# Kernel optimization log

Hardware: AMD Instinct MI355X
Metric: run time of the kernel (lower is better)

The kernel has to match this reference:

```python
import jax, jax.numpy as jnp
import numpy as np

B, T, H = 32, 512, 512
NUM_LAYERS = 2  # outer modules; each nn.GRU itself has NUM_LAYERS internal layers
TOTAL = NUM_LAYERS * NUM_LAYERS  # 4 actual recurrent layers
EPS = 1e-5


def setup_inputs() -> dict:
    key = jax.random.key(0)
    ks = jax.random.split(key, 8)
    s = 1.0 / np.sqrt(H)
    x = jax.random.normal(ks[0], (B, T, H), dtype=jnp.float32)
    # descending lengths in [1, T] (enforce_sorted=True in torch)
    seq_lens = jnp.sort(jax.random.randint(ks[1], (B,), 1, T + 1))[::-1]
    Wih = jax.random.uniform(ks[2], (TOTAL, 3 * H, H), minval=-s, maxval=s)
    Whh = jax.random.uniform(ks[3], (TOTAL, 3 * H, H), minval=-s, maxval=s)
    bih = jax.random.uniform(ks[4], (TOTAL, 3 * H), minval=-s, maxval=s)
    bhh = jax.random.uniform(ks[5], (TOTAL, 3 * H), minval=-s, maxval=s)
    gamma = jnp.ones((NUM_LAYERS, H), jnp.float32)
    beta = jnp.zeros((NUM_LAYERS, H), jnp.float32)
    return {"x": x, "Wih": Wih, "Whh": Whh, "bih": bih, "bhh": bhh,
            "gamma": gamma, "beta": beta, "seq_lens": seq_lens}


def _gru_layer(x, wih, whh, bi, bh):
    # x: [B,T,I]; torch GRU equations (gate order r,z,n)
    xi = jnp.einsum('bti,gi->btg', x, wih) + bi  # [B,T,3H]

    def step(h, xt):
        hh = h @ whh.T + bh
        xr, xz, xn = jnp.split(xt, 3, axis=-1)
        hr, hz, hn = jnp.split(hh, 3, axis=-1)
        r = jax.nn.sigmoid(xr + hr)
        z = jax.nn.sigmoid(xz + hz)
        n = jnp.tanh(xn + r * hn)
        h = (1 - z) * n + z * h
        return h, h

    h0 = jnp.zeros((x.shape[0], whh.shape[1]), x.dtype)
    _, ys = jax.lax.scan(step, h0, jnp.swapaxes(xi, 0, 1))  # [T,B,H]
    return jnp.swapaxes(ys, 0, 1)


def _layernorm(x, g, b):
    mu = jnp.mean(x, axis=-1, keepdims=True)
    var = jnp.mean(jnp.square(x - mu), axis=-1, keepdims=True)
    return (x - mu) * jax.lax.rsqrt(var + EPS) * g + b


def reference(x, Wih, Whh, bih, bhh, gamma, beta, seq_lens):
    # pack_padded_sequence semantics (unidirectional): outputs at valid steps
    # t < len match the full-sequence run; padded steps become zeros after
    # pad_packed_sequence, then LayerNorm is applied to the whole padded tensor.
    mask = (jnp.arange(T)[None, :] < seq_lens[:, None])[:, :, None]  # [B,T,1]
    out = x
    idx = 0
    for l in range(NUM_LAYERS):
        for _k in range(NUM_LAYERS):  # each nn.GRU has NUM_LAYERS internal layers
            out = _gru_layer(out, Wih[idx], Whh[idx], bih[idx], bhh[idx])
            idx += 1
        out = jnp.where(mask, out, 0.0)
        out = _layernorm(out, gamma[l], beta[l])
    return out
```

## Files before the change

### kernel.cpp

```cpp
#include <hip/hip_runtime.h>

typedef unsigned short ushort_t;
typedef __attribute__((ext_vector_type(8))) short short8;
typedef __attribute__((ext_vector_type(4))) float f32x4;

#define B_ 32
#define T_ 512
#define H_ 512
#define CH_ 16

__device__ __forceinline__ float bf2f(ushort_t u) {
  union { unsigned int i; float f; } v; v.i = ((unsigned int)u) << 16; return v.f;
}
__device__ __forceinline__ ushort_t f2bf(float f) {
  union { float fv; unsigned int i; } v; v.fv = f;
  unsigned int x = v.i;
  x += 0x7fffu + ((x >> 16) & 1u);
  return (ushort_t)(x >> 16);
}

__device__ __forceinline__ void poll_row(const int* row, int nf) {
  const int lane = threadIdx.x & 63;
  for (;;) {
    int v = 1;
    if (lane < nf)
      v = __hip_atomic_load(row + lane, __ATOMIC_RELAXED, __HIP_MEMORY_SCOPE_AGENT);
    if (__all(v != 0)) break;
    __builtin_amdgcn_s_sleep(1);
  }
  asm volatile("" ::: "memory");
}

__global__ void prep_w(const float* __restrict__ Wih, const float* __restrict__ Whh,
                       ushort_t* __restrict__ WihBf, ushort_t* __restrict__ WhhBf) {
  int i = blockIdx.x * 256 + threadIdx.x;
  WihBf[i] = f2bf(Wih[i]);
  WhhBf[i] = f2bf(Whh[i]);
}

__global__ void prep_x(const float* __restrict__ x, ushort_t* __restrict__ xA) {
  int i = blockIdx.x * 256 + threadIdx.x;
  int h  = i & (H_ - 1);
  int tb = i >> 9;
  int b  = tb & (B_ - 1);
  int t  = tb >> 5;
  xA[i] = f2bf(x[((size_t)b * T_ + t) * H_ + h]);
}

__device__ void gru_stage(
    const ushort_t* __restrict__ xin, ushort_t* __restrict__ xout,
    const ushort_t* __restrict__ Wih, const ushort_t* __restrict__ Whh,
    const float* __restrict__ bih, const float* __restrict__ bhh,
    ushort_t* __restrict__ hbuf,
    int* __restrict__ selfFl,
    const int* __restrict__ prodFl,
    int prodN, int wg,
    float (*Gx)[33], float (*Gh)[33], float (*hprev)[B_])
{
  const int tid   = threadIdx.x;
  const int lane  = tid & 63;
  const int wave  = tid >> 6;
  const int jb    = wg * CH_;
  const int m16   = lane & 15;
  const int quad  = lane >> 4;
  const int bcol  = (wave & 1) * 16 + m16;

  hprev[tid >> 5][tid & 31]       = 0.0f;
  hprev[8 + (tid >> 5)][tid & 31] = 0.0f;

  const ushort_t* Wsel = (wave < 2) ? Wih : Whh;
  short8 afrag[3][16];
#pragma unroll
  for (int g = 0; g < 3; ++g) {
    const ushort_t* wp = Wsel + (size_t)(g * H_ + jb + m16) * H_ + quad * 8;
#pragma unroll
    for (int kk = 0; kk < 16; ++kk)
      afrag[g][kk] = *(const short8*)(wp + kk * 32);
  }

  const int b0 = tid & 31;
  const int c  = tid >> 5;
  const int c0 = 2 * c, c1 = 2 * c + 1;
  const float bxr0 = bih[0*H_ + jb + c0], bhr0 = bhh[0*H_ + jb + c0];
  const float bxz0 = bih[1*H_ + jb + c0], bhz0 = bhh[1*H_ + jb + c0];
  const float bxn0 = bih[2*H_ + jb + c0], bhn0 = bhh[2*H_ + jb + c0];
  const float bxr1 = bih[0*H_ + jb + c1], bhr1 = bhh[0*H_ + jb + c1];
  const float bxz1 = bih[1*H_ + jb + c1], bhz1 = bhh[1*H_ + jb + c1];
  const float bxn1 = bih[2*H_ + jb + c1], bhn1 = bhh[2*H_ + jb + c1];

  __syncthreads();

  for (int s = 0; s < T_; ++s) {
    f32x4 acc0 = {0.f, 0.f, 0.f, 0.f};
    f32x4 acc1 = acc0, acc2 = acc0;

    if (wave < 2) {
      const ushort_t* src = xin + ((size_t)s * B_ + bcol) * H_ + quad * 8;
      if (prodFl) {
        poll_row(prodFl + s * 32, prodN);
#pragma unroll
        for (int kk = 0; kk < 16; ++kk) {
          const unsigned long long* p = (const unsigned long long*)(src + kk * 32);
          unsigned long long lo = __hip_atomic_load(p,     __ATOMIC_RELAXED, __HIP_MEMORY_SCOPE_AGENT);
          unsigned long long hi = __hip_atomic_load(p + 1, __ATOMIC_RELAXED, __HIP_MEMORY_SCOPE_AGENT);
          union { unsigned long long q[2]; short8 v; } u; u.q[0] = lo; u.q[1] = hi;
          acc0 = __builtin_amdgcn_mfma_f32_16x16x32_bf16(afrag[0][kk], u.v, acc0, 0, 0, 0);
          acc1 = __builtin_amdgcn_mfma_f32_16x16x32_bf16(afrag[1][kk], u.v, acc1, 0, 0, 0);
          acc2 = __builtin_amdgcn_mfma_f32_16x16x32_bf16(afrag[2][kk], u.v, acc2, 0, 0, 0);
        }
      } else {
#pragma unroll
        for (int kk = 0; kk < 16; ++kk) {
          short8 bf = *(const short8*)(src + kk * 32);
          acc0 = __builtin_amdgcn_mfma_f32_16x16x32_bf16(afrag[0][kk], bf, acc0, 0, 0, 0);
          acc1 = __builtin_amdgcn_mfma_f32_16x16x32_bf16(afrag[1][kk], bf, acc1, 0, 0, 0);
          acc2 = __builtin_amdgcn_mfma_f32_16x16x32_bf16(afrag[2][kk], bf, acc2, 0, 0, 0);
        }
      }
    } else {
      if (s > 0) poll_row(selfFl + (s - 1) * 32, 32);
      const ushort_t* src = hbuf + ((size_t)(s & 1) * B_ + bcol) * H_ + quad * 8;
#pragma unroll
      for (int kk = 0; kk < 16; ++kk) {
        const unsigned long long* p = (const unsigned long long*)(src + kk * 32);
        unsigned long long lo = __hip_atomic_load(p,     __ATOMIC_RELAXED, __HIP_MEMORY_SCOPE_AGENT);
        unsigned long long hi = __hip_atomic_load(p + 1, __ATOMIC_RELAXED, __HIP_MEMORY_SCOPE_AGENT);
        union { unsigned long long q[2]; short8 v; } u; u.q[0] = lo; u.q[1] = hi;
        acc0 = __builtin_amdgcn_mfma_f32_16x16x32_bf16(afrag[0][kk], u.v, acc0, 0, 0, 0);
        acc1 = __builtin_amdgcn_mfma_f32_16x16x32_bf16(afrag[1][kk], u.v, acc1, 0, 0, 0);
        acc2 = __builtin_amdgcn_mfma_f32_16x16x32_bf16(afrag[2][kk], u.v, acc2, 0, 0, 0);
      }
    }

    float (*Gd)[33] = (wave < 2) ? Gx : Gh;
#pragma unroll
    for (int r = 0; r < 4; ++r) {
      Gd[ 0 + quad * 4 + r][bcol] = acc0[r];
      Gd[16 + quad * 4 + r][bcol] = acc1[r];
      Gd[32 + quad * 4 + r][bcol] = acc2[r];
    }
    __syncthreads();

    ushort_t* hdst = hbuf + (size_t)((s + 1) & 1) * B_ * H_;
    float hv0, hv1;
    {
      float rr = 1.f / (1.f + __expf(-(Gx[c0][b0] + bxr0 + Gh[c0][b0] + bhr0)));
      float zz = 1.f / (1.f + __expf(-(Gx[16 + c0][b0] + bxz0 + Gh[16 + c0][b0] + bhz0)));
      float nn = tanhf(Gx[32 + c0][b0] + bxn0 + rr * (Gh[32 + c0][b0] + bhn0));
      hv0 = (1.f - zz) * nn + zz * hprev[c0][b0];
      hprev[c0][b0] = hv0;
    }
    {
      float rr = 1.f / (1.f + __expf(-(Gx[c1][b0] + bxr1 + Gh[c1][b0] + bhr1)));
      float zz = 1.f / (1.f + __expf(-(Gx[16 + c1][b0] + bxz1 + Gh[16 + c1][b0] + bhz1)));
      float nn = tanhf(Gx[32 + c1][b0] + bxn1 + rr * (Gh[32 + c1][b0] + bhn1));
      hv1 = (1.f - zz) * nn + zz * hprev[c1][b0];
      hprev[c1][b0] = hv1;
    }
    unsigned int pack = (unsigned int)f2bf(hv0) | ((unsigned int)f2bf(hv1) << 16);
    __hip_atomic_store((unsigned int*)(hdst + (size_t)b0 * H_ + jb + c0), pack,
                       __ATOMIC_RELAXED, __HIP_MEMORY_SCOPE_AGENT);
    __hip_atomic_store((unsigned int*)(xout + ((size_t)s * B_ + b0) * H_ + jb + c0), pack,
                       __ATOMIC_RELAXED, __HIP_MEMORY_SCOPE_AGENT);

    asm volatile("s_waitcnt vmcnt(0)" ::: "memory");
    __syncthreads();
    if (tid == 0)
      __hip_atomic_store(selfFl + s * 32 + wg, 1,
                         __ATOMIC_RELAXED, __HIP_MEMORY_SCOPE_AGENT);
  }
}

__device__ void ln_stage(
    const ushort_t* __restrict__ xin,
    ushort_t* __restrict__ xout_bf,
    float* __restrict__ out_f32,
    const float* __restrict__ gamma, const float* __restrict__ beta,
    const int* __restrict__ seq,
    int* __restrict__ selfFl, const int* __restrict__ prodFl, int prodN, int wg)
{
  const int lane = threadIdx.x & 63;
  const int wv   = threadIdx.x >> 6;
  const int b    = wg * 4 + wv;
  const int len  = seq[b];
  const int h0   = lane * 8;

  float g[8], be[8];
#pragma unroll
  for (int j = 0; j < 8; ++j) { g[j] = gamma[h0 + j]; be[j] = beta[h0 + j]; }

  for (int s = 0; s < T_; ++s) {
    poll_row(prodFl + s * 32, prodN);
    const unsigned long long* p =
        (const unsigned long long*)(xin + ((size_t)s * B_ + b) * H_ + h0);
    unsigned long long lo = __hip_atomic_load(p,     __ATOMIC_RELAXED, __HIP_MEMORY_SCOPE_AGENT);
    unsigned long long hi = __hip_atomic_load(p + 1, __ATOMIC_RELAXED, __HIP_MEMORY_SCOPE_AGENT);
    union { unsigned long long q[2]; ushort_t u[8]; } un; un.q[0] = lo; un.q[1] = hi;
    const bool valid = s < len;
    float v[8];
#pragma unroll
    for (int j = 0; j < 8; ++j) v[j] = valid ? bf2f(un.u[j]) : 0.f;

    float sum = 0.f, sq = 0.f;
#pragma unroll
    for (int j = 0; j < 8; ++j) { sum += v[j]; sq += v[j] * v[j]; }
#pragma unroll
    for (int off = 32; off > 0; off >>= 1) {
      sum += __shfl_xor(sum, off);
      sq  += __shfl_xor(sq, off);
    }
    float mu   = sum * (1.f / H_);
    float var  = sq * (1.f / H_) - mu * mu;
    float rstd = rsqrtf(var + 1e-5f);

    if (xout_bf) {
      union { unsigned long long q[2]; ushort_t u[8]; } o;
#pragma unroll
      for (int j = 0; j < 8; ++j)
        o.u[j] = f2bf((v[j] - mu) * rstd * g[j] + be[j]);
      unsigned long long* q =
          (unsigned long long*)(xout_bf + ((size_t)s * B_ + b) * H_ + h0);
      __hip_atomic_store(q,     o.q[0], __ATOMIC_RELAXED, __HIP_MEMORY_SCOPE_AGENT);
      __hip_atomic_store(q + 1, o.q[1], __ATOMIC_RELAXED, __HIP_MEMORY_SCOPE_AGENT);
      asm volatile("s_waitcnt vmcnt(0)" ::: "memory");
      __syncthreads();
      if (threadIdx.x == 0)
        __hip_atomic_store(selfFl + s * 32 + wg, 1,
                           __ATOMIC_RELAXED, __HIP_MEMORY_SCOPE_AGENT);
    } else {
      float* dst = out_f32 + ((size_t)b * T_ + s) * H_ + h0;
#pragma unroll
      for (int j = 0; j < 8; ++j)
        dst[j] = (v[j] - mu) * rstd * g[j] + be[j];
    }
  }
}

__global__ __launch_bounds__(256, 1) void gru_mega(
    ushort_t* __restrict__ xA, ushort_t* __restrict__ xB,
    ushort_t* __restrict__ xC, ushort_t* __restrict__ xD,
    const ushort_t* __restrict__ WihBf, const ushort_t* __restrict__ WhhBf,
    const float* __restrict__ bih, const float* __restrict__ bhh,
    const float* __restrict__ gamma, const float* __restrict__ beta,
    const int* __restrict__ seq,
    ushort_t* __restrict__ hbase, int* __restrict__ flbase,
    float* __restrict__ out)
{
  __shared__ float Gx[48][33];
  __shared__ float Gh[48][33];
  __shared__ float hprev[CH_][B_];

  const int bid = blockIdx.x;
  const int FS = T_ * 32;
  int* fl0   = flbase;
  int* fl1   = flbase + 1 * FS;
  int* flln0 = flbase + 2 * FS;
  int* fl2   = flbase + 3 * FS;
  int* fl3   = flbase + 4 * FS;
  const int WM = 3 * H_ * H_;
  const int HB = 2 * B_ * H_;

  if (bid < 32) {
    gru_stage(xA, xB, WihBf, WhhBf, bih, bhh,
              hbase, fl0, nullptr, 0, bid, Gx, Gh, hprev);
  } else if (bid < 64) {
    gru_stage(xB, xC, WihBf + WM, WhhBf + WM, bih + 1536, bhh + 1536,
              hbase + HB, fl1, fl0, 32, bid - 32, Gx, Gh, hprev);
  } else if (bid < 72) {
    ln_stage(xC, xD, nullptr, gamma, beta, seq, flln0, fl1, 32, bid - 64);
  } else if (bid < 104) {
    gru_stage(xD, xA, WihBf + 2 * WM, WhhBf + 2 * WM, bih + 2 * 1536, bhh + 2 * 1536,
              hbase + 2 * HB, fl2, flln0, 8, bid - 72, Gx, Gh, hprev);
  } else if (bid < 136) {
    gru_stage(xA, xB, WihBf + 3 * WM, WhhBf + 3 * WM, bih + 3 * 1536, bhh + 3 * 1536,
              hbase + 3 * HB, fl3, fl2, 32, bid - 104, Gx, Gh, hprev);
  } else {
    ln_stage(xB, nullptr, out, gamma + H_, beta + H_, seq,
             nullptr, fl3, 32, bid - 136);
  }
}

#define WIH_OFF 0u
#define WHH_OFF 6291456u
#define XA_OFF  12582912u
#define XB_OFF  29360128u
#define XC_OFF  46137344u
#define XD_OFF  62914560u
#define HB_OFF  79691776u
#define FL_OFF  79953920u

extern "C" void kernel_launch(void* const* d_in, const int* in_sizes, int n_in,
                              void* d_out, int out_size, void* d_ws, size_t ws_size,
                              hipStream_t stream) {
  (void)in_sizes; (void)n_in; (void)out_size; (void)ws_size;
  const float* x     = (const float*)d_in[0];
  const float* Wih   = (const float*)d_in[1];
  const float* Whh   = (const float*)d_in[2];
  const float* bih   = (const float*)d_in[3];
  const float* bhh   = (const float*)d_in[4];
  const float* gamma = (const float*)d_in[5];
  const float* beta  = (const float*)d_in[6];
  const int*   seq   = (const int*)d_in[7];

  char* ws = (char*)d_ws;
  ushort_t* WihBf = (ushort_t*)(ws + WIH_OFF);
  ushort_t* WhhBf = (ushort_t*)(ws + WHH_OFF);
  ushort_t* xA    = (ushort_t*)(ws + XA_OFF);
  ushort_t* xB    = (ushort_t*)(ws + XB_OFF);
  ushort_t* xC    = (ushort_t*)(ws + XC_OFF);
  ushort_t* xD    = (ushort_t*)(ws + XD_OFF);
  ushort_t* hbase = (ushort_t*)(ws + HB_OFF);
  int*      flags = (int*)(ws + FL_OFF);

  hipMemsetAsync(ws + HB_OFF, 0, 262144 + 327680, stream);

  prep_w<<<3145728 / 256, 256, 0, stream>>>(Wih, Whh, WihBf, WhhBf);
  prep_x<<<8388608 / 256, 256, 0, stream>>>(x, xA);

  gru_mega<<<144, 256, 0, stream>>>(xA, xB, xC, xD, WihBf, WhhBf,
                                    bih, bhh, gamma, beta, seq,
                                    hbase, flags, (float*)d_out);
}
```

Before: 4.343 ms.

## Replace block barrier with per-wave flags, batched coherent loads, fast gate math

Each wave now publishes its own completion flag, so the end-of-step __syncthreads is gone and consumers poll 128 flags per step. The shared gate buffers are double-buffered so the next step's writes cannot race the current readers. Producer and recurrent-state reads are issued as 16 batched sc0/sc1 dwordx4 loads, waited on once, instead of pairs of 64-bit atomic loads. Sigmoid and tanh use rcp-based fast approximations, and the hidden state stays in registers. Intermediate buffers are reused to drop one activation buffer, at the cost of more flag memory and slightly less accurate activations.

```diff
diff --git a/kernel.cpp b/kernel.cpp
--- a/kernel.cpp
+++ b/kernel.cpp
@@ -19,14 +19,40 @@
   return (ushort_t)(x >> 16);
 }
 
+__device__ __forceinline__ float fsig(float a) {
+  return __builtin_amdgcn_rcpf(1.f + __expf(-a));
+}
+__device__ __forceinline__ float ftanh(float a) {
+  return 1.f - 2.f * __builtin_amdgcn_rcpf(1.f + __expf(2.f * a));
+}
+
+__device__ __forceinline__ void cload16(short8& dst, const ushort_t* p) {
+  asm volatile("global_load_dwordx4 %0, %1, off sc0 sc1"
+               : "=v"(dst) : "v"(p) : "memory");
+}
+__device__ __forceinline__ void cstore16(const short8& v, ushort_t* p) {
+  asm volatile("global_store_dwordx4 %1, %0, off sc0 sc1"
+               :: "v"(v), "v"(p) : "memory");
+}
+#define WAIT_VM0 asm volatile("s_waitcnt vmcnt(0)" ::: "memory")
+__device__ __forceinline__ void vfence(short8& v) { asm volatile("" : "+v"(v)); }
+
 __device__ __forceinline__ void poll_row(const int* row, int nf) {
   const int lane = threadIdx.x & 63;
-  for (;;) {
-    int v = 1;
-    if (lane < nf)
-      v = __hip_atomic_load(row + lane, __ATOMIC_RELAXED, __HIP_MEMORY_SCOPE_AGENT);
-    if (__all(v != 0)) break;
-    __builtin_amdgcn_s_sleep(1);
+  if (nf > 64) {
+    for (;;) {
+      int a = __hip_atomic_load(row + lane,      __ATOMIC_RELAXED, __HIP_MEMORY_SCOPE_AGENT);
+      int b = __hip_atomic_load(row + 64 + lane, __ATOMIC_RELAXED, __HIP_MEMORY_SCOPE_AGENT);
+      if (__all(a != 0 && b != 0)) break;
+      __builtin_amdgcn_s_sleep(1);
+    }
+  } else {
+    for (;;) {
+      int a = (lane < nf)
+            ? __hip_atomic_load(row + lane, __ATOMIC_RELAXED, __HIP_MEMORY_SCOPE_AGENT) : 1;
+      if (__all(a != 0)) break;
+      __builtin_amdgcn_s_sleep(1);
+    }
   }
   asm volatile("" ::: "memory");
 }
@@ -37,7 +63,6 @@
   WihBf[i] = f2bf(Wih[i]);
   WhhBf[i] = f2bf(Whh[i]);
 }
-
 __global__ void prep_x(const float* __restrict__ x, ushort_t* __restrict__ xA) {
   int i = blockIdx.x * 256 + threadIdx.x;
   int h  = i & (H_ - 1);
@@ -55,7 +80,7 @@
     int* __restrict__ selfFl,
     const int* __restrict__ prodFl,
     int prodN, int wg,
-    float (*Gx)[33], float (*Gh)[33], float (*hprev)[B_])
+    float (*Gbuf)[2][48][33])
 {
   const int tid   = threadIdx.x;
   const int lane  = tid & 63;
@@ -64,9 +89,6 @@
   const int m16   = lane & 15;
   const int quad  = lane >> 4;
   const int bcol  = (wave & 1) * 16 + m16;
-
-  hprev[tid >> 5][tid & 31]       = 0.0f;
-  hprev[8 + (tid >> 5)][tid & 31] = 0.0f;
 
   const ushort_t* Wsel = (wave < 2) ? Wih : Whh;
   short8 afrag[3][16];
@@ -87,26 +109,27 @@
   const float bxr1 = bih[0*H_ + jb + c1], bhr1 = bhh[0*H_ + jb + c1];
   const float bxz1 = bih[1*H_ + jb + c1], bhz1 = bhh[1*H_ + jb + c1];
   const float bxn1 = bih[2*H_ + jb + c1], bhn1 = bhh[2*H_ + jb + c1];
-
-  __syncthreads();
+  float hp0 = 0.f, hp1 = 0.f;
 
   for (int s = 0; s < T_; ++s) {
+    const int p = s & 1;
     f32x4 acc0 = {0.f, 0.f, 0.f, 0.f};
     f32x4 acc1 = acc0, acc2 = acc0;
 
     if (wave < 2) {
       const ushort_t* src = xin + ((size_t)s * B_ + bcol) * H_ + quad * 8;
       if (prodFl) {
-        poll_row(prodFl + s * 32, prodN);
+        poll_row(prodFl + s * prodN, prodN);
+        short8 bfr[16];
+#pragma unroll
+        for (int kk = 0; kk < 16; ++kk) cload16(bfr[kk], src + kk * 32);
+        WAIT_VM0;
 #pragma unroll
         for (int kk = 0; kk < 16; ++kk) {
-          const unsigned long long* p = (const unsigned long long*)(src + kk * 32);
-          unsigned long long lo = __hip_atomic_load(p,     __ATOMIC_RELAXED, __HIP_MEMORY_SCOPE_AGENT);
-          unsigned long long hi = __hip_atomic_load(p + 1, __ATOMIC_RELAXED, __HIP_MEMORY_SCOPE_AGENT);
-          union { unsigned long long q[2]; short8 v; } u; u.q[0] = lo; u.q[1] = hi;
-          acc0 = __builtin_amdgcn_mfma_f32_16x16x32_bf16(afrag[0][kk], u.v, acc0, 0, 0, 0);
-          acc1 = __builtin_amdgcn_mfma_f32_16x16x32_bf16(afrag[1][kk], u.v, acc1, 0, 0, 0);
-          acc2 = __builtin_amdgcn_mfma_f32_16x16x32_bf16(afrag[2][kk], u.v, acc2, 0, 0, 0);
+          vfence(bfr[kk]);
+          acc0 = __builtin_amdgcn_mfma_f32_16x16x32_bf16(afrag[0][kk], bfr[kk], acc0, 0, 0, 0);
+          acc1 = __builtin_amdgcn_mfma_f32_16x16x32_bf16(afrag[1][kk], bfr[kk], acc1, 0, 0, 0);
+          acc2 = __builtin_amdgcn_mfma_f32_16x16x32_bf16(afrag[2][kk], bfr[kk], acc2, 0, 0, 0);
         }
       } else {
 #pragma unroll
@@ -118,21 +141,22 @@
         }
       }
     } else {
-      if (s > 0) poll_row(selfFl + (s - 1) * 32, 32);
-      const ushort_t* src = hbuf + ((size_t)(s & 1) * B_ + bcol) * H_ + quad * 8;
+      if (s > 0) poll_row(selfFl + (s - 1) * 128, 128);
+      const ushort_t* src = hbuf + ((size_t)p * B_ + bcol) * H_ + quad * 8;
+      short8 bfr[16];
+#pragma unroll
+      for (int kk = 0; kk < 16; ++kk) cload16(bfr[kk], src + kk * 32);
+      WAIT_VM0;
 #pragma unroll
       for (int kk = 0; kk < 16; ++kk) {
-        const unsigned long long* p = (const unsigned long long*)(src + kk * 32);
-        unsigned long long lo = __hip_atomic_load(p,     __ATOMIC_RELAXED, __HIP_MEMORY_SCOPE_AGENT);
-        unsigned long long hi = __hip_atomic_load(p + 1, __ATOMIC_RELAXED, __HIP_MEMORY_SCOPE_AGENT);
-        union { unsigned long long q[2]; short8 v; } u; u.q[0] = lo; u.q[1] = hi;
-        acc0 = __builtin_amdgcn_mfma_f32_16x16x32_bf16(afrag[0][kk], u.v, acc0, 0, 0, 0);
-        acc1 = __builtin_amdgcn_mfma_f32_16x16x32_bf16(afrag[1][kk], u.v, acc1, 0, 0, 0);
-        acc2 = __builtin_amdgcn_mfma_f32_16x16x32_bf16(afrag[2][kk], u.v, acc2, 0, 0, 0);
+        vfence(bfr[kk]);
+        acc0 = __builtin_amdgcn_mfma_f32_16x16x32_bf16(afrag[0][kk], bfr[kk], acc0, 0, 0, 0);
+        acc1 = __builtin_amdgcn_mfma_f32_16x16x32_bf16(afrag[1][kk], bfr[kk], acc1, 0, 0, 0);
+        acc2 = __builtin_amdgcn_mfma_f32_16x16x32_bf16(afrag[2][kk], bfr[kk], acc2, 0, 0, 0);
       }
     }
 
-    float (*Gd)[33] = (wave < 2) ? Gx : Gh;
+    float (*Gd)[33] = Gbuf[p][(wave < 2) ? 0 : 1];
 #pragma unroll
     for (int r = 0; r < 4; ++r) {
       Gd[ 0 + quad * 4 + r][bcol] = acc0[r];
@@ -141,32 +165,30 @@
     }
     __syncthreads();
 
-    ushort_t* hdst = hbuf + (size_t)((s + 1) & 1) * B_ * H_;
-    float hv0, hv1;
+    float (*Gx)[33] = Gbuf[p][0];
+    float (*Gh)[33] = Gbuf[p][1];
+    ushort_t* hdst = hbuf + (size_t)(p ^ 1) * B_ * H_;
     {
-      float rr = 1.f / (1.f + __expf(-(Gx[c0][b0] + bxr0 + Gh[c0][b0] + bhr0)));
-      float zz = 1.f / (1.f + __expf(-(Gx[16 + c0][b0] + bxz0 + Gh[16 + c0][b0] + bhz0)));
-      float nn = tanhf(Gx[32 + c0][b0] + bxn0 + rr * (Gh[32 + c0][b0] + bhn0));
-      hv0 = (1.f - zz) * nn + zz * hprev[c0][b0];
-      hprev[c0][b0] = hv0;
+      float rr = fsig(Gx[c0][b0] + bxr0 + Gh[c0][b0] + bhr0);
+      float zz = fsig(Gx[16 + c0][b0] + bxz0 + Gh[16 + c0][b0] + bhz0);
+      float nn = ftanh(Gx[32 + c0][b0] + bxn0 + rr * (Gh[32 + c0][b0] + bhn0));
+      hp0 = (1.f - zz) * nn + zz * hp0;
     }
     {
-      float rr = 1.f / (1.f + __expf(-(Gx[c1][b0] + bxr1 + Gh[c1][b0] + bhr1)));
-      float zz = 1.f / (1.f + __expf(-(Gx[16 + c1][b0] + bxz1 + Gh[16 + c1][b0] + bhz1)));
-      float nn = tanhf(Gx[32 + c1][b0] + bxn1 + rr * (Gh[32 + c1][b0] + bhn1));
-      hv1 = (1.f - zz) * nn + zz * hprev[c1][b0];
-      hprev[c1][b0] = hv1;
-    }
-    unsigned int pack = (unsigned int)f2bf(hv0) | ((unsigned int)f2bf(hv1) << 16);
+      float rr = fsig(Gx[c1][b0] + bxr1 + Gh[c1][b0] + bhr1);
+      float zz = fsig(Gx[16 + c1][b0] + bxz1 + Gh[16 + c1][b0] + bhz1);
+      float nn = ftanh(Gx[32 + c1][b0] + bxn1 + rr * (Gh[32 + c1][b0] + bhn1));
+      hp1 = (1.f - zz) * nn + zz * hp1;
+    }
+    unsigned int pack = (unsigned int)f2bf(hp0) | ((unsigned int)f2bf(hp1) << 16);
     __hip_atomic_store((unsigned int*)(hdst + (size_t)b0 * H_ + jb + c0), pack,
                        __ATOMIC_RELAXED, __HIP_MEMORY_SCOPE_AGENT);
     __hip_atomic_store((unsigned int*)(xout + ((size_t)s * B_ + b0) * H_ + jb + c0), pack,
                        __ATOMIC_RELAXED, __HIP_MEMORY_SCOPE_AGENT);
 
-    asm volatile("s_waitcnt vmcnt(0)" ::: "memory");
-    __syncthreads();
-    if (tid == 0)
-      __hip_atomic_store(selfFl + s * 32 + wg, 1,
+    WAIT_VM0;
+    if (lane == 0)
+      __hip_atomic_store(selfFl + s * 128 + wg * 4 + wave, 1,
                          __ATOMIC_RELAXED, __HIP_MEMORY_SCOPE_AGENT);
   }
 }
@@ -177,7 +199,8 @@
     float* __restrict__ out_f32,
     const float* __restrict__ gamma, const float* __restrict__ beta,
     const int* __restrict__ seq,
-    int* __restrict__ selfFl, const int* __restrict__ prodFl, int prodN, int wg)
+    int* __restrict__ selfFl,
+    const int* __restrict__ prodFl, int prodN, int wg)
 {
   const int lane = threadIdx.x & 63;
   const int wv   = threadIdx.x >> 6;
@@ -190,16 +213,15 @@
   for (int j = 0; j < 8; ++j) { g[j] = gamma[h0 + j]; be[j] = beta[h0 + j]; }
 
   for (int s = 0; s < T_; ++s) {
-    poll_row(prodFl + s * 32, prodN);
-    const unsigned long long* p =
-        (const unsigned long long*)(xin + ((size_t)s * B_ + b) * H_ + h0);
-    unsigned long long lo = __hip_atomic_load(p,     __ATOMIC_RELAXED, __HIP_MEMORY_SCOPE_AGENT);
-    unsigned long long hi = __hip_atomic_load(p + 1, __ATOMIC_RELAXED, __HIP_MEMORY_SCOPE_AGENT);
-    union { unsigned long long q[2]; ushort_t u[8]; } un; un.q[0] = lo; un.q[1] = hi;
+    poll_row(prodFl + s * prodN, prodN);
+    short8 raw;
+    cload16(raw, xin + ((size_t)s * B_ + b) * H_ + h0);
+    WAIT_VM0;
+    vfence(raw);
     const bool valid = s < len;
     float v[8];
 #pragma unroll
-    for (int j = 0; j < 8; ++j) v[j] = valid ? bf2f(un.u[j]) : 0.f;
+    for (int j = 0; j < 8; ++j) v[j] = valid ? bf2f((ushort_t)raw[j]) : 0.f;
 
     float sum = 0.f, sq = 0.f;
 #pragma unroll
@@ -214,18 +236,14 @@
     float rstd = rsqrtf(var + 1e-5f);
 
     if (xout_bf) {
-      union { unsigned long long q[2]; ushort_t u[8]; } o;
+      short8 o;
 #pragma unroll
       for (int j = 0; j < 8; ++j)
-        o.u[j] = f2bf((v[j] - mu) * rstd * g[j] + be[j]);
-      unsigned long long* q =
-          (unsigned long long*)(xout_bf + ((size_t)s * B_ + b) * H_ + h0);
-      __hip_atomic_store(q,     o.q[0], __ATOMIC_RELAXED, __HIP_MEMORY_SCOPE_AGENT);
-      __hip_atomic_store(q + 1, o.q[1], __ATOMIC_RELAXED, __HIP_MEMORY_SCOPE_AGENT);
-      asm volatile("s_waitcnt vmcnt(0)" ::: "memory");
-      __syncthreads();
-      if (threadIdx.x == 0)
-        __hip_atomic_store(selfFl + s * 32 + wg, 1,
+        o[j] = (short)f2bf((v[j] - mu) * rstd * g[j] + be[j]);
+      cstore16(o, xout_bf + ((size_t)s * B_ + b) * H_ + h0);
+      WAIT_VM0;
+      if (lane == 0)
+        __hip_atomic_store(selfFl + s * 32 + b, 1,
                            __ATOMIC_RELAXED, __HIP_MEMORY_SCOPE_AGENT);
     } else {
       float* dst = out_f32 + ((size_t)b * T_ + s) * H_ + h0;
@@ -237,8 +255,7 @@
 }
 
 __global__ __launch_bounds__(256, 1) void gru_mega(
-    ushort_t* __restrict__ xA, ushort_t* __restrict__ xB,
-    ushort_t* __restrict__ xC, ushort_t* __restrict__ xD,
+    ushort_t* __restrict__ xA, ushort_t* __restrict__ xB, ushort_t* __restrict__ xC,
     const ushort_t* __restrict__ WihBf, const ushort_t* __restrict__ WhhBf,
     const float* __restrict__ bih, const float* __restrict__ bhh,
     const float* __restrict__ gamma, const float* __restrict__ beta,
@@ -246,37 +263,36 @@
     ushort_t* __restrict__ hbase, int* __restrict__ flbase,
     float* __restrict__ out)
 {
-  __shared__ float Gx[48][33];
-  __shared__ float Gh[48][33];
-  __shared__ float hprev[CH_][B_];
+  __shared__ float Gbuf[2][2][48][33];
 
   const int bid = blockIdx.x;
-  const int FS = T_ * 32;
+  const int GRUF = T_ * 128;
+  const int LNF  = T_ * 32;
   int* fl0   = flbase;
-  int* fl1   = flbase + 1 * FS;
-  int* flln0 = flbase + 2 * FS;
-  int* fl2   = flbase + 3 * FS;
-  int* fl3   = flbase + 4 * FS;
-  const int WM = 3 * H_ * H_;
-  const int HB = 2 * B_ * H_;
+  int* fl1   = flbase + GRUF;
+  int* flln0 = flbase + 2 * GRUF;
+  int* fl2   = flbase + 2 * GRUF + LNF;
+  int* fl3   = flbase + 3 * GRUF + LNF;
+  const int WM  = 3 * H_ * H_;
+  const int HBL = 2 * B_ * H_;
 
   if (bid < 32) {
     gru_stage(xA, xB, WihBf, WhhBf, bih, bhh,
-              hbase, fl0, nullptr, 0, bid, Gx, Gh, hprev);
+              hbase, fl0, nullptr, 0, bid, Gbuf);
   } else if (bid < 64) {
     gru_stage(xB, xC, WihBf + WM, WhhBf + WM, bih + 1536, bhh + 1536,
-              hbase + HB, fl1, fl0, 32, bid - 32, Gx, Gh, hprev);
+              hbase + HBL, fl1, fl0, 128, bid - 32, Gbuf);
   } else if (bid < 72) {
-    ln_stage(xC, xD, nullptr, gamma, beta, seq, flln0, fl1, 32, bid - 64);
+    ln_stage(xC, xA, nullptr, gamma, beta, seq, flln0, fl1, 128, bid - 64);
   } else if (bid < 104) {
-    gru_stage(xD, xA, WihBf + 2 * WM, WhhBf + 2 * WM, bih + 2 * 1536, bhh + 2 * 1536,
-              hbase + 2 * HB, fl2, flln0, 8, bid - 72, Gx, Gh, hprev);
+    gru_stage(xA, xC, WihBf + 2 * WM, WhhBf + 2 * WM, bih + 2 * 1536, bhh + 2 * 1536,
+              hbase + 2 * HBL, fl2, flln0, 32, bid - 72, Gbuf);
   } else if (bid < 136) {
-    gru_stage(xA, xB, WihBf + 3 * WM, WhhBf + 3 * WM, bih + 3 * 1536, bhh + 3 * 1536,
-              hbase + 3 * HB, fl3, fl2, 32, bid - 104, Gx, Gh, hprev);
+    gru_stage(xC, xB, WihBf + 3 * WM, WhhBf + 3 * WM, bih + 3 * 1536, bhh + 3 * 1536,
+              hbase + 3 * HBL, fl3, fl2, 128, bid - 104, Gbuf);
   } else {
     ln_stage(xB, nullptr, out, gamma + H_, beta + H_, seq,
-             nullptr, fl3, 32, bid - 136);
+             nullptr, fl3, 128, bid - 136);
   }
 }
 
@@ -285,9 +301,8 @@
 #define XA_OFF  12582912u
 #define XB_OFF  29360128u
 #define XC_OFF  46137344u
-#define XD_OFF  62914560u
-#define HB_OFF  79691776u
-#define FL_OFF  79953920u
+#define HB_OFF  62914560u
+#define FL_OFF  63176704u
 
 extern "C" void kernel_launch(void* const* d_in, const int* in_sizes, int n_in,
                               void* d_out, int out_size, void* d_ws, size_t ws_size,
@@ -308,16 +323,15 @@
   ushort_t* xA    = (ushort_t*)(ws + XA_OFF);
   ushort_t* xB    = (ushort_t*)(ws + XB_OFF);
   ushort_t* xC    = (ushort_t*)(ws + XC_OFF);
-  ushort_t* xD    = (ushort_t*)(ws + XD_OFF);
   ushort_t* hbase = (ushort_t*)(ws + HB_OFF);
   int*      flags = (int*)(ws + FL_OFF);
 
-  hipMemsetAsync(ws + HB_OFF, 0, 262144 + 327680, stream);
+  hipMemsetAsync(ws + HB_OFF, 0, 262144u + 1114112u, stream);
 
   prep_w<<<3145728 / 256, 256, 0, stream>>>(Wih, Whh, WihBf, WhhBf);
   prep_x<<<8388608 / 256, 256, 0, stream>>>(x, xA);
 
-  gru_mega<<<144, 256, 0, stream>>>(xA, xB, xC, xD, WihBf, WhhBf,
+  gru_mega<<<144, 256, 0, stream>>>(xA, xB, xC, WihBf, WhhBf,
                                     bih, bhh, gamma, beta, seq,
                                     hbase, flags, (float*)d_out);
 }
```

New measurement: 3.891 ms. -10.4%, faster.
